# Optimization experiments

Measured on AMD Instinct MI355X. Metric: run time of the kernel, lower is better.

Reference implementation:

```python
import jax, jax.numpy as jnp
import numpy as np

B, S, D, H = 2, 2048, 1024, 16
HD = D // H
LAMBDA_INIT = 0.8
EPS = 1e-5


def setup_inputs() -> dict:
    key = jax.random.key(0)
    ks = jax.random.split(key, 14)
    f32 = jnp.float32
    return {
        "inputs": jax.random.normal(ks[0], (B, S, D), f32),
        "attention_mask": jnp.ones((B, S), f32),
        "Wq": jax.random.normal(ks[1], (D, 2 * D), f32) * 0.02,
        "Wk": jax.random.normal(ks[2], (D, 2 * D), f32) * 0.02,
        "Wv": jax.random.normal(ks[3], (D, D), f32) * 0.02,
        "Wo": jax.random.normal(ks[4], (D, D), f32) * 0.02,
        "lam_q1": jax.random.normal(ks[5], (HD,), f32) * 0.1,
        "lam_q2": jax.random.normal(ks[6], (HD,), f32) * 0.1,
        "lam_k1": jax.random.normal(ks[7], (HD,), f32) * 0.1,
        "lam_k2": jax.random.normal(ks[8], (HD,), f32) * 0.1,
        "gn_weight": jnp.ones((D,), f32),
        "gn_bias": jnp.zeros((D,), f32),
        "memory_gate": jax.random.normal(ks[9], (1, H, 1, HD), f32),
        "mem": jnp.zeros((1, H, HD, HD), f32),
        "z": jnp.ones((1, H, HD, 1), f32),
    }


def reference(inputs, attention_mask, Wq, Wk, Wv, Wo, lam_q1, lam_q2, lam_k1, lam_k2,
              gn_weight, gn_bias, memory_gate, mem, z):
    Bv, Sv, Dv = inputs.shape
    scale = 1.0 / jnp.sqrt(jnp.float32(HD))
    q = (inputs @ Wq).reshape(Bv, Sv, H, 2 * HD).transpose(0, 2, 1, 3)  # B,H,S,2hd
    k = (inputs @ Wk).reshape(Bv, Sv, H, 2 * HD).transpose(0, 2, 1, 3)
    v = (inputs @ Wv).reshape(Bv, Sv, H, HD).transpose(0, 2, 1, 3)      # B,H,S,hd
    Q1, Q2 = q[..., :HD], q[..., HD:]
    K1, K2 = k[..., :HD], k[..., HD:]
    pos = jnp.arange(Sv, dtype=jnp.float32)
    slopes = 2.0 ** (-8.0 * jnp.arange(1, H + 1, dtype=jnp.float32) / H)
    alibi = slopes[None, :, None, None] * (pos[:, None] - pos[None, :])[None, None]  # 1,H,S,S
    causal = jnp.triu(jnp.full((Sv, Sv), -1e9, jnp.float32), k=1)
    pad = (1.0 - attention_mask)[:, None, None, :] * -1e9  # B,1,1,S
    def attn(Q, K):
        s = jnp.einsum('bhqd,bhkd->bhqk', Q, K) * scale - alibi + causal + pad
        return jax.nn.softmax(s, axis=-1)
    w1 = attn(Q1, K1)
    w2 = attn(Q2, K2)
    lam = jnp.exp(jnp.dot(lam_q1, lam_k1)) - jnp.exp(jnp.dot(lam_q2, lam_k2)) + LAMBDA_INIT
    diff_w = w1 - lam * w2  # B,H,S,S
    # linear-attention memory read (mem update is dead code w.r.t. output)
    sigma_q = jax.nn.elu(Q1) + 1.0
    mem_values = (sigma_q @ mem) / (sigma_q @ z)  # B,H,S,hd
    gate = jax.nn.sigmoid(memory_gate)
    out = gate * mem_values + (1.0 - gate) * jnp.einsum('bhqk,bhkd->bhqd', diff_w, v)
    # GroupNorm(num_groups=H) over channels-first layout: per (head) group stats over (hd, S)
    x = out.transpose(0, 1, 3, 2)  # B,H,hd,S
    mu = x.mean(axis=(2, 3), keepdims=True)
    var = ((x - mu) ** 2).mean(axis=(2, 3), keepdims=True)
    xn = (x - mu) / jnp.sqrt(var + EPS)
    xn = xn * gn_weight.reshape(1, H, HD, 1) + gn_bias.reshape(1, H, HD, 1)
    y = xn.transpose(0, 3, 1, 2).reshape(Bv, Sv, H * HD) * (1.0 - LAMBDA_INIT)
    return y @ Wo
```

## Files before the change

kernel.cpp:

```cpp
#include <hip/hip_runtime.h>
#include <stdint.h>

#define B_ 2
#define S_ 2048
#define D_ 1024
#define H_ 16
#define HD_ 64
#define NC_ 5120

typedef unsigned short ushort_t;
typedef __bf16 bf16x8_t __attribute__((ext_vector_type(8)));
typedef unsigned short us8 __attribute__((ext_vector_type(8)));
typedef float f32x4 __attribute__((ext_vector_type(4)));
typedef unsigned int u32x4 __attribute__((ext_vector_type(4)));

using gq_t = const unsigned int __attribute__((address_space(1)));
using lq_t = unsigned int __attribute__((address_space(3)));

__device__ __forceinline__ unsigned short f2bf(float f) {
    unsigned u = __builtin_bit_cast(unsigned, f);
    u += 0x7fffu + ((u >> 16) & 1u);
    return (unsigned short)(u >> 16);
}
__device__ __forceinline__ float bf2f(unsigned short h) {
    unsigned u = ((unsigned)h) << 16;
    return __builtin_bit_cast(float, u);
}
__device__ __forceinline__ unsigned cvt_pk_bf16(float lo, float hi) {
    unsigned r;
    asm("v_cvt_pk_bf16_f32 %0, %1, %2" : "=v"(r) : "v"(lo), "v"(hi));
    return r;
}
__device__ __forceinline__ f32x4 mfma16(us8 a, us8 b, f32x4 c) {
    return __builtin_amdgcn_mfma_f32_16x16x32_bf16(
        __builtin_bit_cast(bf16x8_t, a), __builtin_bit_cast(bf16x8_t, b), c, 0, 0, 0);
}
__device__ __forceinline__ void gload16(const void* g, void* l) {
    __builtin_amdgcn_global_load_lds((gq_t*)g, (lq_t*)l, 16, 0, 0);
}
__device__ __forceinline__ int invpi(int p) {
    return (p & 0x20) | ((p & 0x0C) << 1) | ((p & 0x10) >> 2) | (p & 3);
}

__global__ __launch_bounds__(256) void k_convert_x(const float* __restrict__ X,
                                                   ushort_t* __restrict__ Xb) {
    int i = (blockIdx.x * 256 + threadIdx.x) * 4;
    float4 v = *reinterpret_cast<const float4*>(X + i);
    ushort4 o;
    o.x = f2bf(v.x); o.y = f2bf(v.y); o.z = f2bf(v.z); o.w = f2bf(v.w);
    *reinterpret_cast<ushort4*>(Xb + i) = o;
}

__global__ __launch_bounds__(256) void k_transpose_w(const float* __restrict__ W,
                                                     ushort_t* __restrict__ Bt,
                                                     int N, int n_base) {
    __shared__ float lds[64 * 65];
    int n0 = blockIdx.x * 64, k0 = blockIdx.y * 64;
    int t = threadIdx.x;
#pragma unroll
    for (int i = 0; i < 16; i++) {
        int idx = i * 256 + t;
        int r = idx >> 6, c = idx & 63;
        lds[c * 65 + r] = W[(size_t)(k0 + r) * N + (n0 + c)];
    }
    __syncthreads();
#pragma unroll
    for (int i = 0; i < 16; i++) {
        int idx = i * 256 + t;
        int nn = idx >> 6, k = idx & 63;
        Bt[(size_t)(n_base + n0 + nn) * 1024 + (k0 + k)] = f2bf(lds[nn * 65 + k]);
    }
}

__device__ __forceinline__ void gemm_tile(const ushort_t* __restrict__ A,
                                          const ushort_t* __restrict__ Bt,
                                          int m0, int n0,
                                          ushort_t* ldsA, ushort_t* ldsB,
                                          f32x4 acc[4][4]) {
    const int K = 1024;
    int t = threadIdx.x;
    int w = t >> 6, l = t & 63;
    int wr = (w >> 1) * 64, wc = (w & 1) * 64;
    int lo16 = l & 15, lg = l >> 4;
#pragma unroll
    for (int m = 0; m < 4; m++)
#pragma unroll
        for (int n = 0; n < 4; n++) acc[m][n] = f32x4{0.f, 0.f, 0.f, 0.f};

    for (int k0 = 0; k0 < K; k0 += 64) {
#pragma unroll
        for (int i = 0; i < 4; i++) {
            int c = i * 256 + t;
            int row = c >> 3, co = (c & 7) * 8;
            gload16(A + (size_t)(m0 + row) * K + k0 + co, ldsA + (size_t)c * 8);
            gload16(Bt + (size_t)(n0 + row) * K + k0 + co, ldsB + (size_t)c * 8);
        }
        __syncthreads();
#pragma unroll
        for (int kk = 0; kk < 2; kk++) {
            us8 af[4], bfr[4];
#pragma unroll
            for (int m = 0; m < 4; m++)
                af[m] = *(const us8*)(ldsA + (wr + m * 16 + lo16) * 64 + kk * 32 + lg * 8);
#pragma unroll
            for (int n = 0; n < 4; n++)
                bfr[n] = *(const us8*)(ldsB + (wc + n * 16 + lo16) * 64 + kk * 32 + lg * 8);
#pragma unroll
            for (int m = 0; m < 4; m++)
#pragma unroll
                for (int n = 0; n < 4; n++)
                    acc[m][n] = mfma16(af[m], bfr[n], acc[m][n]);
        }
        __syncthreads();
    }
}

__global__ __launch_bounds__(256) void k_gemm_qkv(const ushort_t* __restrict__ Xb,
                                                  const ushort_t* __restrict__ Wt,
                                                  ushort_t* __restrict__ C) {
    __shared__ __align__(16) ushort_t ldsA[128 * 64];
    __shared__ __align__(16) ushort_t ldsB[128 * 64];
    f32x4 acc[4][4];
    int m0 = blockIdx.y * 128, n0 = blockIdx.x * 128;
    gemm_tile(Xb, Wt, m0, n0, ldsA, ldsB, acc);
    int t = threadIdx.x, w = t >> 6, l = t & 63;
    int wr = (w >> 1) * 64, wc = (w & 1) * 64, lo16 = l & 15, lg = l >> 4;
#pragma unroll
    for (int m = 0; m < 4; m++)
#pragma unroll
        for (int n = 0; n < 4; n++)
#pragma unroll
            for (int r = 0; r < 4; r++)
                C[(size_t)(m0 + wr + m * 16 + lg * 4 + r) * NC_ + (n0 + wc + n * 16 + lo16)] =
                    f2bf(acc[m][n][r]);
}

__global__ __launch_bounds__(256) void k_gemm_out(const ushort_t* __restrict__ Yb,
                                                  const ushort_t* __restrict__ Wot,
                                                  float* __restrict__ Out) {
    __shared__ __align__(16) ushort_t ldsA[128 * 64];
    __shared__ __align__(16) ushort_t ldsB[128 * 64];
    f32x4 acc[4][4];
    int m0 = blockIdx.y * 128, n0 = blockIdx.x * 128;
    gemm_tile(Yb, Wot, m0, n0, ldsA, ldsB, acc);
    int t = threadIdx.x, w = t >> 6, l = t & 63;
    int wr = (w >> 1) * 64, wc = (w & 1) * 64, lo16 = l & 15, lg = l >> 4;
#pragma unroll
    for (int m = 0; m < 4; m++)
#pragma unroll
        for (int n = 0; n < 4; n++)
#pragma unroll
            for (int r = 0; r < 4; r++)
                Out[(size_t)(m0 + wr + m * 16 + lg * 4 + r) * 1024 + (n0 + wc + n * 16 + lo16)] =
                    acc[m][n][r];
}

__global__ __launch_bounds__(256) void k_transpose_v(const ushort_t* __restrict__ C,
                                                     ushort_t* __restrict__ Vt) {
    __shared__ ushort_t lds[64 * 72];
    int bh = blockIdx.x, s0 = blockIdx.y * 64;
    int b = bh >> 4, h = bh & 15;
    const ushort_t* src = C + (size_t)(b * S_ + s0) * NC_ + 4096 + h * 64;
    ushort_t* dst = Vt + (size_t)bh * HD_ * S_ + s0;
    int t = threadIdx.x;
#pragma unroll
    for (int i = 0; i < 16; i++) {
        int idx = i * 256 + t;
        int s = idx >> 6, d = idx & 63;
        lds[d * 72 + s] = src[(size_t)s * NC_ + d];
    }
    __syncthreads();
#pragma unroll
    for (int i = 0; i < 16; i++) {
        int idx = i * 256 + t;
        int d = idx >> 6, s = idx & 63;
        dst[(size_t)d * S_ + s] = lds[d * 72 + s];
    }
}

__global__ __launch_bounds__(256, 3) void k_attn(
    const ushort_t* __restrict__ Cg, const ushort_t* __restrict__ Vtg,
    const float* __restrict__ mask,
    const float* __restrict__ lam_q1, const float* __restrict__ lam_q2,
    const float* __restrict__ lam_k1, const float* __restrict__ lam_k2,
    const float* __restrict__ mgate, const float* __restrict__ memp,
    const float* __restrict__ zp, float* __restrict__ Oatt, float* __restrict__ stats) {
    __shared__ __align__(16) ushort_t smem[2 * 12288];
    __shared__ __align__(16) float ldsAdj[2][64];
    ushort_t* ldsM = smem;

    int bx = blockIdx.x;
    int xcd = bx & 7, slot = bx >> 3;
    int sub = slot & 3;
    int qt = 31 - (slot >> 2);
    int h = (sub & 1) ? (15 - xcd) : xcd;
    int b = sub >> 1;
    int bh = b * 16 + h;
    int q0 = qt * 64;
    int t = threadIdx.x, w = t >> 6, l = t & 63;
    int lo16 = l & 15, lg = l >> 4;

    const ushort_t* Cb  = Cg + (size_t)(b * S_) * NC_;
    const ushort_t* Qp  = Cb + h * 128;
    const ushort_t* Kp  = Cb + 2048 + h * 128;
    const ushort_t* Vt  = Vtg + (size_t)bh * HD_ * S_;

    int qrowA = q0 + w * 16 + lo16;
    us8 q1f[2], q2f[2];
    q1f[0] = *(const us8*)(Qp + (size_t)qrowA * NC_ + lg * 8);
    q1f[1] = *(const us8*)(Qp + (size_t)qrowA * NC_ + 32 + lg * 8);
    q2f[0] = *(const us8*)(Qp + (size_t)qrowA * NC_ + 64 + lg * 8);
    q2f[1] = *(const us8*)(Qp + (size_t)qrowA * NC_ + 96 + lg * 8);

    float la = 0.f, lb = 0.f;
    for (int i = 0; i < HD_; i++) { la += lam_q1[i] * lam_k1[i]; lb += lam_q2[i] * lam_k2[i]; }
    float lam = __expf(la) - __expf(lb) + 0.8f;

    const float LOG2E = 1.4426950408889634f;
    float slope2 = exp2f(-0.5f * (float)(h + 1)) * LOG2E;
    const float scale2 = 0.125f * LOG2E;

    int qcol = q0 + w * 16 + lo16;
    float qterm = -slope2 * (float)qcol - 8.0f;

    int koff[4];
#pragma unroll
    for (int n = 0; n < 4; n++) koff[n] = ((n >> 1) << 5) | (lg << 3) | ((n & 1) << 2);

    int fs = (int)floorf(((float)q0 - 63.0f - 60.0f / slope2) * (1.0f / 64.0f));
    if (fs < 0) fs = 0;

    int sx0 = (lg ^ (lo16 & 7)) * 8;
    int sx1 = ((4 + lg) ^ (lo16 & 7)) * 8;

    f32x4 o1[5], o2[5];
#pragma unroll
    for (int n = 0; n < 5; n++) { o1[n] = f32x4{0, 0, 0, 0}; o2[n] = f32x4{0, 0, 0, 0}; }

    const us8 ones8 = {0x3F80, 0x3F80, 0x3F80, 0x3F80, 0x3F80, 0x3F80, 0x3F80, 0x3F80};

    auto stage = [&](int buf, int kv0) {
        ushort_t* base = smem + buf * 12288;
#pragma unroll
        for (int i = 0; i < 2; i++) {
            int c = i * 256 + t, row = c >> 3;
            int co = ((c & 7) ^ (row & 7)) * 8;
            int kvsrc = kv0 + invpi(row);
            const ushort_t* krow = Kp + (size_t)kvsrc * NC_;
            gload16(krow + co, base + c * 8);
            gload16(krow + 64 + co, base + 4096 + c * 8);
            gload16(Vt + (size_t)row * S_ + kv0 + co, base + 8192 + c * 8);
        }
        if (t < 64) {
            int kvloc = invpi(t);
            ldsAdj[buf][t] = (1.f - mask[(size_t)b * S_ + kv0 + kvloc]) * -1.4426950e9f +
                             slope2 * (float)(kv0 + kvloc);
        }
    };

    auto score_pack = [&](const ushort_t* ldsK, const us8* qf, bool diag, int kv0,
                          const f32x4 (&madj)[4], us8 (&pa)[2]) {
        f32x4 s[4];
#pragma unroll
        for (int n = 0; n < 4; n++) s[n] = f32x4{0, 0, 0, 0};
        __builtin_amdgcn_s_setprio(1);
#pragma unroll
        for (int kk = 0; kk < 2; kk++) {
            int sxk = kk ? sx1 : sx0;
#pragma unroll
            for (int n = 0; n < 4; n++) {
                us8 kf = *(const us8*)(ldsK + (n * 16 + lo16) * 64 + sxk);
                s[n] = mfma16(kf, qf[kk], s[n]);
            }
        }
        __builtin_amdgcn_s_setprio(0);
#pragma unroll
        for (int n = 0; n < 4; n++)
#pragma unroll
            for (int r = 0; r < 4; r++)
                s[n][r] = fmaf(s[n][r], scale2, madj[n][r] + qterm);
        if (diag) {
#pragma unroll
            for (int n = 0; n < 4; n++) {
                int kvn = kv0 + koff[n];
#pragma unroll
                for (int r = 0; r < 4; r++)
                    if (kvn + r > qcol) s[n][r] = -1e30f;
            }
        }
        float p[4][4];
#pragma unroll
        for (int n = 0; n < 4; n++)
#pragma unroll
            for (int r = 0; r < 4; r++) p[n][r] = __builtin_amdgcn_exp2f(s[n][r]);
#pragma unroll
        for (int kk = 0; kk < 2; kk++) {
            u32x4 u;
            u[0] = cvt_pk_bf16(p[2 * kk][0], p[2 * kk][1]);
            u[1] = cvt_pk_bf16(p[2 * kk][2], p[2 * kk][3]);
            u[2] = cvt_pk_bf16(p[2 * kk + 1][0], p[2 * kk + 1][1]);
            u[3] = cvt_pk_bf16(p[2 * kk + 1][2], p[2 * kk + 1][3]);
            pa[kk] = __builtin_bit_cast(us8, u);
        }
    };

    int cur = 0;
    stage(0, qt * 64);
    __syncthreads();
    for (int step = qt; step >= fs; --step) {
        if (step - 1 >= fs) stage(cur ^ 1, (step - 1) * 64);
        int kv0 = step * 64;
        ushort_t* base = smem + cur * 12288;
        const ushort_t* ldsV = base + 8192;

        f32x4 madj[4];
#pragma unroll
        for (int n = 0; n < 4; n++)
            madj[n] = *(const f32x4*)(&ldsAdj[cur][n * 16 + lg * 4]);

        bool diag = (step == qt);
        us8 pa1[2], pa2[2];
        score_pack(base, q1f, diag, kv0, madj, pa1);
        score_pack(base + 4096, q2f, diag, kv0, madj, pa2);

        __builtin_amdgcn_s_setprio(1);
#pragma unroll
        for (int kk = 0; kk < 2; kk++) {
            o1[4] = mfma16(pa1[kk], ones8, o1[4]);
            o2[4] = mfma16(pa2[kk], ones8, o2[4]);
            int sxk = kk ? sx1 : sx0;
#pragma unroll
            for (int n = 0; n < 4; n++) {
                us8 vf = *(const us8*)(ldsV + (n * 16 + lo16) * 64 + sxk);
                o1[n] = mfma16(pa1[kk], vf, o1[n]);
                o2[n] = mfma16(pa2[kk], vf, o2[n]);
            }
        }
        __builtin_amdgcn_s_setprio(0);
        __syncthreads();
        cur ^= 1;
    }

    for (int i = t; i < 80 * 64; i += 256) {
        int n = i >> 6, kd = i & 63;
        float v = 0.f;
        if (n < 64) v = memp[((size_t)h * 64 + kd) * 64 + n];
        else if (n == 64) v = zp[h * 64 + kd];
        ldsM[i] = f2bf(v);
    }
    __syncthreads();

    us8 sf[2];
#pragma unroll
    for (int kk = 0; kk < 2; kk++) {
#pragma unroll
        for (int j = 0; j < 8; j++) {
            float x = bf2f(q1f[kk][j]);
            float e = (x > 0.f) ? x : (__expf(x) - 1.f);
            sf[kk][j] = f2bf(e + 1.f);
        }
    }
    f32x4 mv[5];
#pragma unroll
    for (int n = 0; n < 5; n++) mv[n] = f32x4{0, 0, 0, 0};
#pragma unroll
    for (int kk = 0; kk < 2; kk++)
#pragma unroll
        for (int n = 0; n < 5; n++) {
            us8 mb = *(const us8*)(ldsM + (n * 16 + lo16) * 64 + kk * 32 + lg * 8);
            mv[n] = mfma16(sf[kk], mb, mv[n]);
        }
    float denom[4];
#pragma unroll
    for (int r = 0; r < 4; r++) denom[r] = __shfl(mv[4][r], lg * 16);

    float gsum = 0.f, gsq = 0.f;
#pragma unroll
    for (int n = 0; n < 4; n++) {
        int d = n * 16 + lo16;
        float gate = 1.f / (1.f + __expf(-mgate[h * HD_ + d]));
#pragma unroll
        for (int r = 0; r < 4; r++) {
            int q = q0 + w * 16 + lg * 4 + r;
            float dmv = mv[n][r] / denom[r];
            float oa = o1[n][r] / o1[4][r] - lam * (o2[n][r] / o2[4][r]);
            float val = gate * dmv + (1.f - gate) * oa;
            Oatt[((size_t)bh * S_ + q) * HD_ + d] = val;
            gsum += val;
            gsq += val * val;
        }
    }
#pragma unroll
    for (int off = 1; off < 64; off <<= 1) {
        gsum += __shfl_xor(gsum, off);
        gsq += __shfl_xor(gsq, off);
    }
    if (l == 0) {
        atomicAdd(&stats[bh * 2 + 0], gsum);
        atomicAdd(&stats[bh * 2 + 1], gsq);
    }
}

__global__ __launch_bounds__(256) void k_norm(const float* __restrict__ Oatt,
                                              const float* __restrict__ stats,
                                              const float* __restrict__ gw,
                                              const float* __restrict__ gb,
                                              ushort_t* __restrict__ Yb) {
    int i4 = (blockIdx.x * 256 + threadIdx.x) * 4;
    int bh = i4 >> 17;
    int rest = i4 & 131071;
    int s = rest >> 6, d = rest & 63;
    int b = bh >> 4, h = bh & 15;
    float mu = stats[bh * 2] * (1.f / 131072.f);
    float var = stats[bh * 2 + 1] * (1.f / 131072.f) - mu * mu;
    float rstd = rsqrtf(var + 1e-5f);
    float4 v = *reinterpret_cast<const float4*>(Oatt + i4);
    int c = h * 64 + d;
    ushort4 o;
    o.x = f2bf(((v.x - mu) * rstd * gw[c + 0] + gb[c + 0]) * 0.2f);
    o.y = f2bf(((v.y - mu) * rstd * gw[c + 1] + gb[c + 1]) * 0.2f);
    o.z = f2bf(((v.z - mu) * rstd * gw[c + 2] + gb[c + 2]) * 0.2f);
    o.w = f2bf(((v.w - mu) * rstd * gw[c + 3] + gb[c + 3]) * 0.2f);
    *reinterpret_cast<ushort4*>(Yb + ((size_t)(b * S_ + s)) * 1024 + c) = o;
}

extern "C" void kernel_launch(void* const* d_in, const int* in_sizes, int n_in,
                              void* d_out, int out_size, void* d_ws, size_t ws_size,
                              hipStream_t stream) {
    const float* X      = (const float*)d_in[0];
    const float* mask   = (const float*)d_in[1];
    const float* Wq     = (const float*)d_in[2];
    const float* Wk     = (const float*)d_in[3];
    const float* Wv     = (const float*)d_in[4];
    const float* Wo     = (const float*)d_in[5];
    const float* lam_q1 = (const float*)d_in[6];
    const float* lam_q2 = (const float*)d_in[7];
    const float* lam_k1 = (const float*)d_in[8];
    const float* lam_k2 = (const float*)d_in[9];
    const float* gw     = (const float*)d_in[10];
    const float* gb     = (const float*)d_in[11];
    const float* mgate  = (const float*)d_in[12];
    const float* memp   = (const float*)d_in[13];
    const float* zp     = (const float*)d_in[14];

    char* p = (char*)d_ws;
    auto alloc = [&](size_t bytes) -> char* {
        char* r = p;
        p += (bytes + 255) & ~(size_t)255;
        return r;
    };
    ushort_t* Xb  = (ushort_t*)alloc((size_t)4096 * 1024 * 2);
    ushort_t* Wt  = (ushort_t*)alloc((size_t)5120 * 1024 * 2);
    ushort_t* Wot = (ushort_t*)alloc((size_t)1024 * 1024 * 2);
    ushort_t* C   = (ushort_t*)alloc((size_t)4096 * NC_ * 2);
    ushort_t* Vt  = (ushort_t*)alloc((size_t)B_ * H_ * S_ * HD_ * 2);
    float*    Oat = (float*)alloc((size_t)B_ * H_ * S_ * HD_ * 4);
    ushort_t* Yb  = (ushort_t*)alloc((size_t)4096 * 1024 * 2);
    float*    st  = (float*)alloc(256);

    k_convert_x<<<4096, 256, 0, stream>>>(X, Xb);
    k_transpose_w<<<dim3(32, 16), 256, 0, stream>>>(Wq, Wt, 2048, 0);
    k_transpose_w<<<dim3(32, 16), 256, 0, stream>>>(Wk, Wt, 2048, 2048);
    k_transpose_w<<<dim3(16, 16), 256, 0, stream>>>(Wv, Wt, 1024, 4096);
    k_transpose_w<<<dim3(16, 16), 256, 0, stream>>>(Wo, Wot, 1024, 0);
    k_gemm_qkv<<<dim3(40, 32), 256, 0, stream>>>(Xb, Wt, C);
    k_transpose_v<<<dim3(32, 32), 256, 0, stream>>>(C, Vt);
    hipMemsetAsync(st, 0, 64 * sizeof(float), stream);
    k_attn<<<1024, 256, 0, stream>>>(C, Vt, mask, lam_q1, lam_q2,
                                     lam_k1, lam_k2, mgate, memp, zp, Oat, st);
    k_norm<<<4096, 256, 0, stream>>>(Oat, st, gw, gb, Yb);
    k_gemm_out<<<dim3(8, 32), 256, 0, stream>>>(Yb, Wot, (float*)d_out);
}
```

Before: 204.6 us.

## Process two adjacent query tiles per attention block to reuse staged K/V

Each attention block now handles two consecutive 64-row query tiles, sharing every staged K/V tile in LDS between both tiles' score and PV MFMAs. This halves the grid to 512 blocks and roughly halves K/V global loads and staging. The cost is doubled accumulator registers, with occupancy lowered to 2 blocks per CU, and fewer blocks to balance the causal triangle.

Result: no change. 205.2 us (+0.3%).

```diff
diff --git a/kernel.cpp b/kernel.cpp
--- a/kernel.cpp
+++ b/kernel.cpp
@@ -178,7 +178,7 @@
     }
 }
 
-__global__ __launch_bounds__(256, 3) void k_attn(
+__global__ __launch_bounds__(256, 2) void k_attn(
     const ushort_t* __restrict__ Cg, const ushort_t* __restrict__ Vtg,
     const float* __restrict__ mask,
     const float* __restrict__ lam_q1, const float* __restrict__ lam_q2,
@@ -192,11 +192,12 @@
     int bx = blockIdx.x;
     int xcd = bx & 7, slot = bx >> 3;
     int sub = slot & 3;
-    int qt = 31 - (slot >> 2);
+    int qp = 15 - (slot >> 2);
     int h = (sub & 1) ? (15 - xcd) : xcd;
     int b = sub >> 1;
     int bh = b * 16 + h;
-    int q0 = qt * 64;
+    int qta = 2 * qp, qtb = 2 * qp + 1;
+    int q0a = qta * 64, q0b = qtb * 64;
     int t = threadIdx.x, w = t >> 6, l = t & 63;
     int lo16 = l & 15, lg = l >> 4;
 
@@ -205,12 +206,17 @@
     const ushort_t* Kp  = Cb + 2048 + h * 128;
     const ushort_t* Vt  = Vtg + (size_t)bh * HD_ * S_;
 
-    int qrowA = q0 + w * 16 + lo16;
-    us8 q1f[2], q2f[2];
-    q1f[0] = *(const us8*)(Qp + (size_t)qrowA * NC_ + lg * 8);
-    q1f[1] = *(const us8*)(Qp + (size_t)qrowA * NC_ + 32 + lg * 8);
-    q2f[0] = *(const us8*)(Qp + (size_t)qrowA * NC_ + 64 + lg * 8);
-    q2f[1] = *(const us8*)(Qp + (size_t)qrowA * NC_ + 96 + lg * 8);
+    int qrA = q0a + w * 16 + lo16;
+    int qrB = q0b + w * 16 + lo16;
+    us8 qa1f[2], qa2f[2], qb1f[2], qb2f[2];
+    qa1f[0] = *(const us8*)(Qp + (size_t)qrA * NC_ + lg * 8);
+    qa1f[1] = *(const us8*)(Qp + (size_t)qrA * NC_ + 32 + lg * 8);
+    qa2f[0] = *(const us8*)(Qp + (size_t)qrA * NC_ + 64 + lg * 8);
+    qa2f[1] = *(const us8*)(Qp + (size_t)qrA * NC_ + 96 + lg * 8);
+    qb1f[0] = *(const us8*)(Qp + (size_t)qrB * NC_ + lg * 8);
+    qb1f[1] = *(const us8*)(Qp + (size_t)qrB * NC_ + 32 + lg * 8);
+    qb2f[0] = *(const us8*)(Qp + (size_t)qrB * NC_ + 64 + lg * 8);
+    qb2f[1] = *(const us8*)(Qp + (size_t)qrB * NC_ + 96 + lg * 8);
 
     float la = 0.f, lb = 0.f;
     for (int i = 0; i < HD_; i++) { la += lam_q1[i] * lam_k1[i]; lb += lam_q2[i] * lam_k2[i]; }
@@ -220,22 +226,27 @@
     float slope2 = exp2f(-0.5f * (float)(h + 1)) * LOG2E;
     const float scale2 = 0.125f * LOG2E;
 
-    int qcol = q0 + w * 16 + lo16;
-    float qterm = -slope2 * (float)qcol - 8.0f;
+    int qcolA = q0a + w * 16 + lo16;
+    int qcolB = q0b + w * 16 + lo16;
+    float qtermA = -slope2 * (float)qcolA - 8.0f;
+    float qtermB = -slope2 * (float)qcolB - 8.0f;
 
     int koff[4];
 #pragma unroll
     for (int n = 0; n < 4; n++) koff[n] = ((n >> 1) << 5) | (lg << 3) | ((n & 1) << 2);
 
-    int fs = (int)floorf(((float)q0 - 63.0f - 60.0f / slope2) * (1.0f / 64.0f));
+    int fs = (int)floorf(((float)q0a - 63.0f - 60.0f / slope2) * (1.0f / 64.0f));
     if (fs < 0) fs = 0;
 
     int sx0 = (lg ^ (lo16 & 7)) * 8;
     int sx1 = ((4 + lg) ^ (lo16 & 7)) * 8;
 
-    f32x4 o1[5], o2[5];
-#pragma unroll
-    for (int n = 0; n < 5; n++) { o1[n] = f32x4{0, 0, 0, 0}; o2[n] = f32x4{0, 0, 0, 0}; }
+    f32x4 oa1[5], oa2[5], ob1[5], ob2[5];
+#pragma unroll
+    for (int n = 0; n < 5; n++) {
+        oa1[n] = f32x4{0, 0, 0, 0}; oa2[n] = f32x4{0, 0, 0, 0};
+        ob1[n] = f32x4{0, 0, 0, 0}; ob2[n] = f32x4{0, 0, 0, 0};
+    }
 
     const us8 ones8 = {0x3F80, 0x3F80, 0x3F80, 0x3F80, 0x3F80, 0x3F80, 0x3F80, 0x3F80};
 
@@ -258,11 +269,12 @@
         }
     };
 
-    auto score_pack = [&](const ushort_t* ldsK, const us8* qf, bool diag, int kv0,
-                          const f32x4 (&madj)[4], us8 (&pa)[2]) {
-        f32x4 s[4];
-#pragma unroll
-        for (int n = 0; n < 4; n++) s[n] = f32x4{0, 0, 0, 0};
+    auto score2 = [&](const ushort_t* ldsK, const us8 (&qfB)[2], const us8 (&qfA)[2],
+                      bool actA, bool diagB, bool diagA, int kv0,
+                      const f32x4 (&madj)[4], us8 (&paB)[2], us8 (&paA)[2]) {
+        f32x4 sB[4], sA[4];
+#pragma unroll
+        for (int n = 0; n < 4; n++) { sB[n] = f32x4{0, 0, 0, 0}; sA[n] = f32x4{0, 0, 0, 0}; }
         __builtin_amdgcn_s_setprio(1);
 #pragma unroll
         for (int kk = 0; kk < 2; kk++) {
@@ -270,7 +282,8 @@
 #pragma unroll
             for (int n = 0; n < 4; n++) {
                 us8 kf = *(const us8*)(ldsK + (n * 16 + lo16) * 64 + sxk);
-                s[n] = mfma16(kf, qf[kk], s[n]);
+                sB[n] = mfma16(kf, qfB[kk], sB[n]);
+                if (actA) sA[n] = mfma16(kf, qfA[kk], sA[n]);
             }
         }
         __builtin_amdgcn_s_setprio(0);
@@ -278,36 +291,64 @@
         for (int n = 0; n < 4; n++)
 #pragma unroll
             for (int r = 0; r < 4; r++)
-                s[n][r] = fmaf(s[n][r], scale2, madj[n][r] + qterm);
-        if (diag) {
+                sB[n][r] = fmaf(sB[n][r], scale2, madj[n][r] + qtermB);
+        if (diagB) {
 #pragma unroll
             for (int n = 0; n < 4; n++) {
                 int kvn = kv0 + koff[n];
 #pragma unroll
                 for (int r = 0; r < 4; r++)
-                    if (kvn + r > qcol) s[n][r] = -1e30f;
-            }
-        }
-        float p[4][4];
+                    if (kvn + r > qcolB) sB[n][r] = -1e30f;
+            }
+        }
 #pragma unroll
         for (int n = 0; n < 4; n++)
 #pragma unroll
-            for (int r = 0; r < 4; r++) p[n][r] = __builtin_amdgcn_exp2f(s[n][r]);
+            for (int r = 0; r < 4; r++) sB[n][r] = __builtin_amdgcn_exp2f(sB[n][r]);
 #pragma unroll
         for (int kk = 0; kk < 2; kk++) {
             u32x4 u;
-            u[0] = cvt_pk_bf16(p[2 * kk][0], p[2 * kk][1]);
-            u[1] = cvt_pk_bf16(p[2 * kk][2], p[2 * kk][3]);
-            u[2] = cvt_pk_bf16(p[2 * kk + 1][0], p[2 * kk + 1][1]);
-            u[3] = cvt_pk_bf16(p[2 * kk + 1][2], p[2 * kk + 1][3]);
-            pa[kk] = __builtin_bit_cast(us8, u);
+            u[0] = cvt_pk_bf16(sB[2 * kk][0], sB[2 * kk][1]);
+            u[1] = cvt_pk_bf16(sB[2 * kk][2], sB[2 * kk][3]);
+            u[2] = cvt_pk_bf16(sB[2 * kk + 1][0], sB[2 * kk + 1][1]);
+            u[3] = cvt_pk_bf16(sB[2 * kk + 1][2], sB[2 * kk + 1][3]);
+            paB[kk] = __builtin_bit_cast(us8, u);
+        }
+        if (actA) {
+#pragma unroll
+            for (int n = 0; n < 4; n++)
+#pragma unroll
+                for (int r = 0; r < 4; r++)
+                    sA[n][r] = fmaf(sA[n][r], scale2, madj[n][r] + qtermA);
+            if (diagA) {
+#pragma unroll
+                for (int n = 0; n < 4; n++) {
+                    int kvn = kv0 + koff[n];
+#pragma unroll
+                    for (int r = 0; r < 4; r++)
+                        if (kvn + r > qcolA) sA[n][r] = -1e30f;
+                }
+            }
+#pragma unroll
+            for (int n = 0; n < 4; n++)
+#pragma unroll
+                for (int r = 0; r < 4; r++) sA[n][r] = __builtin_amdgcn_exp2f(sA[n][r]);
+#pragma unroll
+            for (int kk = 0; kk < 2; kk++) {
+                u32x4 u;
+                u[0] = cvt_pk_bf16(sA[2 * kk][0], sA[2 * kk][1]);
+                u[1] = cvt_pk_bf16(sA[2 * kk][2], sA[2 * kk][3]);
+                u[2] = cvt_pk_bf16(sA[2 * kk + 1][0], sA[2 * kk + 1][1]);
+                u[3] = cvt_pk_bf16(sA[2 * kk + 1][2], sA[2 * kk + 1][3]);
+                paA[kk] = __builtin_bit_cast(us8, u);
+            }
         }
     };
 
     int cur = 0;
-    stage(0, qt * 64);
+    stage(0, qtb * 64);
     __syncthreads();
-    for (int step = qt; step >= fs; --step) {
+    for (int step = qtb; step >= fs; --step) {
         if (step - 1 >= fs) stage(cur ^ 1, (step - 1) * 64);
         int kv0 = step * 64;
         ushort_t* base = smem + cur * 12288;
@@ -318,22 +359,32 @@
         for (int n = 0; n < 4; n++)
             madj[n] = *(const f32x4*)(&ldsAdj[cur][n * 16 + lg * 4]);
 
-        bool diag = (step == qt);
-        us8 pa1[2], pa2[2];
-        score_pack(base, q1f, diag, kv0, madj, pa1);
-        score_pack(base + 4096, q2f, diag, kv0, madj, pa2);
+        bool diagB = (step == qtb);
+        bool actA = (step <= qta);
+        bool diagA = (step == qta);
+        us8 pb1[2], pb2[2], pa1[2], pa2[2];
+        score2(base, qb1f, qa1f, actA, diagB, diagA, kv0, madj, pb1, pa1);
+        score2(base + 4096, qb2f, qa2f, actA, diagB, diagA, kv0, madj, pb2, pa2);
 
         __builtin_amdgcn_s_setprio(1);
 #pragma unroll
         for (int kk = 0; kk < 2; kk++) {
-            o1[4] = mfma16(pa1[kk], ones8, o1[4]);
-            o2[4] = mfma16(pa2[kk], ones8, o2[4]);
+            ob1[4] = mfma16(pb1[kk], ones8, ob1[4]);
+            ob2[4] = mfma16(pb2[kk], ones8, ob2[4]);
+            if (actA) {
+                oa1[4] = mfma16(pa1[kk], ones8, oa1[4]);
+                oa2[4] = mfma16(pa2[kk], ones8, oa2[4]);
+            }
             int sxk = kk ? sx1 : sx0;
 #pragma unroll
             for (int n = 0; n < 4; n++) {
                 us8 vf = *(const us8*)(ldsV + (n * 16 + lo16) * 64 + sxk);
-                o1[n] = mfma16(pa1[kk], vf, o1[n]);
-                o2[n] = mfma16(pa2[kk], vf, o2[n]);
+                ob1[n] = mfma16(pb1[kk], vf, ob1[n]);
+                ob2[n] = mfma16(pb2[kk], vf, ob2[n]);
+                if (actA) {
+                    oa1[n] = mfma16(pa1[kk], vf, oa1[n]);
+                    oa2[n] = mfma16(pa2[kk], vf, oa2[n]);
+                }
             }
         }
         __builtin_amdgcn_s_setprio(0);
@@ -350,46 +401,54 @@
     }
     __syncthreads();
 
-    us8 sf[2];
-#pragma unroll
-    for (int kk = 0; kk < 2; kk++) {
-#pragma unroll
-        for (int j = 0; j < 8; j++) {
-            float x = bf2f(q1f[kk][j]);
-            float e = (x > 0.f) ? x : (__expf(x) - 1.f);
-            sf[kk][j] = f2bf(e + 1.f);
-        }
-    }
-    f32x4 mv[5];
-#pragma unroll
-    for (int n = 0; n < 5; n++) mv[n] = f32x4{0, 0, 0, 0};
-#pragma unroll
-    for (int kk = 0; kk < 2; kk++)
-#pragma unroll
-        for (int n = 0; n < 5; n++) {
-            us8 mb = *(const us8*)(ldsM + (n * 16 + lo16) * 64 + kk * 32 + lg * 8);
-            mv[n] = mfma16(sf[kk], mb, mv[n]);
-        }
-    float denom[4];
-#pragma unroll
-    for (int r = 0; r < 4; r++) denom[r] = __shfl(mv[4][r], lg * 16);
-
     float gsum = 0.f, gsq = 0.f;
-#pragma unroll
-    for (int n = 0; n < 4; n++) {
-        int d = n * 16 + lo16;
-        float gate = 1.f / (1.f + __expf(-mgate[h * HD_ + d]));
-#pragma unroll
-        for (int r = 0; r < 4; r++) {
-            int q = q0 + w * 16 + lg * 4 + r;
-            float dmv = mv[n][r] / denom[r];
-            float oa = o1[n][r] / o1[4][r] - lam * (o2[n][r] / o2[4][r]);
-            float val = gate * dmv + (1.f - gate) * oa;
-            Oatt[((size_t)bh * S_ + q) * HD_ + d] = val;
-            gsum += val;
-            gsq += val * val;
-        }
-    }
+
+    auto epilogue_tile = [&](const us8 (&q1f)[2], const f32x4 (&o1)[5], const f32x4 (&o2)[5],
+                             int q0) {
+        us8 sf[2];
+#pragma unroll
+        for (int kk = 0; kk < 2; kk++) {
+#pragma unroll
+            for (int j = 0; j < 8; j++) {
+                float x = bf2f(q1f[kk][j]);
+                float e = (x > 0.f) ? x : (__expf(x) - 1.f);
+                sf[kk][j] = f2bf(e + 1.f);
+            }
+        }
+        f32x4 mv[5];
+#pragma unroll
+        for (int n = 0; n < 5; n++) mv[n] = f32x4{0, 0, 0, 0};
+#pragma unroll
+        for (int kk = 0; kk < 2; kk++)
+#pragma unroll
+            for (int n = 0; n < 5; n++) {
+                us8 mb = *(const us8*)(ldsM + (n * 16 + lo16) * 64 + kk * 32 + lg * 8);
+                mv[n] = mfma16(sf[kk], mb, mv[n]);
+            }
+        float denom[4];
+#pragma unroll
+        for (int r = 0; r < 4; r++) denom[r] = __shfl(mv[4][r], lg * 16);
+
+#pragma unroll
+        for (int n = 0; n < 4; n++) {
+            int d = n * 16 + lo16;
+            float gate = 1.f / (1.f + __expf(-mgate[h * HD_ + d]));
+#pragma unroll
+            for (int r = 0; r < 4; r++) {
+                int q = q0 + w * 16 + lg * 4 + r;
+                float dmv = mv[n][r] / denom[r];
+                float oa = o1[n][r] / o1[4][r] - lam * (o2[n][r] / o2[4][r]);
+                float val = gate * dmv + (1.f - gate) * oa;
+                Oatt[((size_t)bh * S_ + q) * HD_ + d] = val;
+                gsum += val;
+                gsq += val * val;
+            }
+        }
+    };
+
+    epilogue_tile(qa1f, oa1, oa2, q0a);
+    epilogue_tile(qb1f, ob1, ob2, q0b);
+
 #pragma unroll
     for (int off = 1; off < 64; off <<= 1) {
         gsum += __shfl_xor(gsum, off);
@@ -466,8 +525,8 @@
     k_gemm_qkv<<<dim3(40, 32), 256, 0, stream>>>(Xb, Wt, C);
     k_transpose_v<<<dim3(32, 32), 256, 0, stream>>>(C, Vt);
     hipMemsetAsync(st, 0, 64 * sizeof(float), stream);
-    k_attn<<<1024, 256, 0, stream>>>(C, Vt, mask, lam_q1, lam_q2,
-                                     lam_k1, lam_k2, mgate, memp, zp, Oat, st);
+    k_attn<<<512, 256, 0, stream>>>(C, Vt, mask, lam_q1, lam_q2,
+                                    lam_k1, lam_k2, mgate, memp, zp, Oat, st);
     k_norm<<<4096, 256, 0, stream>>>(Oat, st, gw, gb, Yb);
     k_gemm_out<<<dim3(8, 32), 256, 0, stream>>>(Yb, Wot, (float*)d_out);
 }
```

## Fuse GroupNorm into output GEMM A-load and merge weight transposes

Applied to the files above, without the earlier changes.

Four weight-transpose launches are merged into one kernel that dispatches on block index. The separate GroupNorm kernel and its bf16 Yb buffer are removed: the output GEMM now reads fp32 attention output directly, normalizes it, converts to bf16 and stores into LDS as its A tile. This drops a full write and read of the normalized activations and two launches. In exchange, each of the 8 column blocks repeats the normalization for the same rows and reads fp32 (twice the bytes of bf16), and the A-tile load becomes synchronous register traffic instead of an async global-to-LDS load.

New measurement: 211.1 us. 3.2% more time.

```diff
diff --git a/kernel.cpp b/kernel.cpp
--- a/kernel.cpp
+++ b/kernel.cpp
@@ -51,11 +51,20 @@
     *reinterpret_cast<ushort4*>(Xb + i) = o;
 }
 
-__global__ __launch_bounds__(256) void k_transpose_w(const float* __restrict__ W,
-                                                     ushort_t* __restrict__ Bt,
-                                                     int N, int n_base) {
+__global__ __launch_bounds__(256) void k_transpose_all(const float* __restrict__ Wq,
+                                                       const float* __restrict__ Wk,
+                                                       const float* __restrict__ Wv,
+                                                       const float* __restrict__ Wo,
+                                                       ushort_t* __restrict__ Wt,
+                                                       ushort_t* __restrict__ Wot) {
     __shared__ float lds[64 * 65];
-    int n0 = blockIdx.x * 64, k0 = blockIdx.y * 64;
+    int bx = blockIdx.x;
+    const float* W; ushort_t* dst; int N, nbase, x;
+    if (bx < 32)      { W = Wq; dst = Wt;  N = 2048; nbase = 0;    x = bx; }
+    else if (bx < 64) { W = Wk; dst = Wt;  N = 2048; nbase = 2048; x = bx - 32; }
+    else if (bx < 80) { W = Wv; dst = Wt;  N = 1024; nbase = 4096; x = bx - 64; }
+    else              { W = Wo; dst = Wot; N = 1024; nbase = 0;    x = bx - 80; }
+    int n0 = x * 64, k0 = blockIdx.y * 64;
     int t = threadIdx.x;
 #pragma unroll
     for (int i = 0; i < 16; i++) {
@@ -68,7 +77,7 @@
     for (int i = 0; i < 16; i++) {
         int idx = i * 256 + t;
         int nn = idx >> 6, k = idx & 63;
-        Bt[(size_t)(n_base + n0 + nn) * 1024 + (k0 + k)] = f2bf(lds[nn * 65 + k]);
+        dst[(size_t)(nbase + n0 + nn) * 1024 + (k0 + k)] = f2bf(lds[nn * 65 + k]);
     }
 }
 
@@ -135,16 +144,76 @@
                     f2bf(acc[m][n][r]);
 }
 
-__global__ __launch_bounds__(256) void k_gemm_out(const ushort_t* __restrict__ Yb,
+__global__ __launch_bounds__(256) void k_gemm_out(const float* __restrict__ Oat,
+                                                  const float* __restrict__ stats,
+                                                  const float* __restrict__ gw,
+                                                  const float* __restrict__ gb,
                                                   const ushort_t* __restrict__ Wot,
                                                   float* __restrict__ Out) {
     __shared__ __align__(16) ushort_t ldsA[128 * 64];
     __shared__ __align__(16) ushort_t ldsB[128 * 64];
+    const int K = 1024;
+    int t = threadIdx.x;
+    int w = t >> 6, l = t & 63;
+    int wr = (w >> 1) * 64, wc = (w & 1) * 64;
+    int lo16 = l & 15, lg = l >> 4;
+    int m0 = blockIdx.y * 128, n0 = blockIdx.x * 128;
     f32x4 acc[4][4];
-    int m0 = blockIdx.y * 128, n0 = blockIdx.x * 128;
-    gemm_tile(Yb, Wot, m0, n0, ldsA, ldsB, acc);
-    int t = threadIdx.x, w = t >> 6, l = t & 63;
-    int wr = (w >> 1) * 64, wc = (w & 1) * 64, lo16 = l & 15, lg = l >> 4;
+#pragma unroll
+    for (int m = 0; m < 4; m++)
+#pragma unroll
+        for (int n = 0; n < 4; n++) acc[m][n] = f32x4{0.f, 0.f, 0.f, 0.f};
+
+    for (int k0 = 0; k0 < K; k0 += 64) {
+#pragma unroll
+        for (int i = 0; i < 4; i++) {
+            int c = i * 256 + t;
+            int row = c >> 3, cg = (c & 7) * 8;
+            gload16(Wot + (size_t)(n0 + row) * K + k0 + cg, ldsB + (size_t)c * 8);
+            int grow = m0 + row;
+            int k = k0 + cg;
+            int b = grow >> 11, s = grow & 2047;
+            int h = k >> 6, d = k & 63;
+            int bh = b * 16 + h;
+            float mu = stats[bh * 2] * (1.f / 131072.f);
+            float var = stats[bh * 2 + 1] * (1.f / 131072.f) - mu * mu;
+            float rstd = rsqrtf(var + 1e-5f);
+            const float* src = Oat + ((size_t)bh * S_ + s) * HD_ + d;
+            float4 v0 = *(const float4*)src;
+            float4 v1 = *(const float4*)(src + 4);
+            float4 g0 = *(const float4*)(gw + k);
+            float4 g1 = *(const float4*)(gw + k + 4);
+            float4 c0 = *(const float4*)(gb + k);
+            float4 c1 = *(const float4*)(gb + k + 4);
+            us8 o;
+            o[0] = f2bf((fmaf((v0.x - mu) * rstd, g0.x, c0.x)) * 0.2f);
+            o[1] = f2bf((fmaf((v0.y - mu) * rstd, g0.y, c0.y)) * 0.2f);
+            o[2] = f2bf((fmaf((v0.z - mu) * rstd, g0.z, c0.z)) * 0.2f);
+            o[3] = f2bf((fmaf((v0.w - mu) * rstd, g0.w, c0.w)) * 0.2f);
+            o[4] = f2bf((fmaf((v1.x - mu) * rstd, g1.x, c1.x)) * 0.2f);
+            o[5] = f2bf((fmaf((v1.y - mu) * rstd, g1.y, c1.y)) * 0.2f);
+            o[6] = f2bf((fmaf((v1.z - mu) * rstd, g1.z, c1.z)) * 0.2f);
+            o[7] = f2bf((fmaf((v1.w - mu) * rstd, g1.w, c1.w)) * 0.2f);
+            *(us8*)(ldsA + (size_t)c * 8) = o;
+        }
+        __syncthreads();
+#pragma unroll
+        for (int kk = 0; kk < 2; kk++) {
+            us8 af[4], bfr[4];
+#pragma unroll
+            for (int m = 0; m < 4; m++)
+                af[m] = *(const us8*)(ldsA + (wr + m * 16 + lo16) * 64 + kk * 32 + lg * 8);
+#pragma unroll
+            for (int n = 0; n < 4; n++)
+                bfr[n] = *(const us8*)(ldsB + (wc + n * 16 + lo16) * 64 + kk * 32 + lg * 8);
+#pragma unroll
+            for (int m = 0; m < 4; m++)
+#pragma unroll
+                for (int n = 0; n < 4; n++)
+                    acc[m][n] = mfma16(af[m], bfr[n], acc[m][n]);
+        }
+        __syncthreads();
+    }
 #pragma unroll
     for (int m = 0; m < 4; m++)
 #pragma unroll
@@ -399,29 +468,6 @@
         atomicAdd(&stats[bh * 2 + 0], gsum);
         atomicAdd(&stats[bh * 2 + 1], gsq);
     }
-}
-
-__global__ __launch_bounds__(256) void k_norm(const float* __restrict__ Oatt,
-                                              const float* __restrict__ stats,
-                                              const float* __restrict__ gw,
-                                              const float* __restrict__ gb,
-                                              ushort_t* __restrict__ Yb) {
-    int i4 = (blockIdx.x * 256 + threadIdx.x) * 4;
-    int bh = i4 >> 17;
-    int rest = i4 & 131071;
-    int s = rest >> 6, d = rest & 63;
-    int b = bh >> 4, h = bh & 15;
-    float mu = stats[bh * 2] * (1.f / 131072.f);
-    float var = stats[bh * 2 + 1] * (1.f / 131072.f) - mu * mu;
-    float rstd = rsqrtf(var + 1e-5f);
-    float4 v = *reinterpret_cast<const float4*>(Oatt + i4);
-    int c = h * 64 + d;
-    ushort4 o;
-    o.x = f2bf(((v.x - mu) * rstd * gw[c + 0] + gb[c + 0]) * 0.2f);
-    o.y = f2bf(((v.y - mu) * rstd * gw[c + 1] + gb[c + 1]) * 0.2f);
-    o.z = f2bf(((v.z - mu) * rstd * gw[c + 2] + gb[c + 2]) * 0.2f);
-    o.w = f2bf(((v.w - mu) * rstd * gw[c + 3] + gb[c + 3]) * 0.2f);
-    *reinterpret_cast<ushort4*>(Yb + ((size_t)(b * S_ + s)) * 1024 + c) = o;
 }
 
 extern "C" void kernel_launch(void* const* d_in, const int* in_sizes, int n_in,
@@ -455,19 +501,14 @@
     ushort_t* C   = (ushort_t*)alloc((size_t)4096 * NC_ * 2);
     ushort_t* Vt  = (ushort_t*)alloc((size_t)B_ * H_ * S_ * HD_ * 2);
     float*    Oat = (float*)alloc((size_t)B_ * H_ * S_ * HD_ * 4);
-    ushort_t* Yb  = (ushort_t*)alloc((size_t)4096 * 1024 * 2);
     float*    st  = (float*)alloc(256);
 
     k_convert_x<<<4096, 256, 0, stream>>>(X, Xb);
-    k_transpose_w<<<dim3(32, 16), 256, 0, stream>>>(Wq, Wt, 2048, 0);
-    k_transpose_w<<<dim3(32, 16), 256, 0, stream>>>(Wk, Wt, 2048, 2048);
-    k_transpose_w<<<dim3(16, 16), 256, 0, stream>>>(Wv, Wt, 1024, 4096);
-    k_transpose_w<<<dim3(16, 16), 256, 0, stream>>>(Wo, Wot, 1024, 0);
+    k_transpose_all<<<dim3(96, 16), 256, 0, stream>>>(Wq, Wk, Wv, Wo, Wt, Wot);
     k_gemm_qkv<<<dim3(40, 32), 256, 0, stream>>>(Xb, Wt, C);
     k_transpose_v<<<dim3(32, 32), 256, 0, stream>>>(C, Vt);
     hipMemsetAsync(st, 0, 64 * sizeof(float), stream);
     k_attn<<<1024, 256, 0, stream>>>(C, Vt, mask, lam_q1, lam_q2,
                                      lam_k1, lam_k2, mgate, memp, zp, Oat, st);
-    k_norm<<<4096, 256, 0, stream>>>(Oat, st, gw, gb, Yb);
-    k_gemm_out<<<dim3(8, 32), 256, 0, stream>>>(Yb, Wot, (float*)d_out);
-}
+    k_gemm_out<<<dim3(8, 32), 256, 0, stream>>>(Oat, st, gw, gb, Wot, (float*)d_out);
+}
```
